# Performance work log

Hardware: AMD Instinct MI355X
Metric: run time of the kernel (lower is better)

## Reference

```python
import jax, jax.numpy as jnp
import numpy as np

DIM = 512
HEADS = 4
DH = 128          # dim_head
CHUNK = 16        # chunk_size
MAX_LR = 0.01     # default_adaptive_step_transform max_lr
EPS = 1e-6        # flax RMSNorm epsilon


def setup_inputs() -> dict:
    key = jax.random.key(0)
    ks = jax.random.split(key, 8)
    B, S = 2, 2048
    dim_inner = HEADS * DH
    seq = jax.random.normal(ks[0], (B, S, DIM), jnp.float32)
    store_norm_scale = jnp.ones((DIM,), jnp.float32)               # RMSNorm scale
    W_kv = (jax.random.normal(ks[1], (DIM, 2 * dim_inner)) * 0.02).astype(jnp.float32)
    W_step = (jax.random.normal(ks[2], (DIM, HEADS)) * 0.02).astype(jnp.float32)
    W_mom = (jax.random.normal(ks[3], (DIM, HEADS)) * 0.02).astype(jnp.float32)
    W_decay = (jax.random.normal(ks[4], (DIM, HEADS)) * 0.02).astype(jnp.float32)
    # past memory-MLP weights, shared init expanded to (b, h, dh, dh)
    w0 = jnp.broadcast_to((jax.random.normal(ks[5], (DH, DH)) * 0.02).astype(jnp.float32), (B, HEADS, DH, DH)) + 0.0
    w1 = jnp.broadcast_to((jax.random.normal(ks[6], (DH, DH)) * 0.02).astype(jnp.float32), (B, HEADS, DH, DH)) + 0.0
    return {"seq": seq, "store_norm_scale": store_norm_scale, "W_kv": W_kv,
            "W_step": W_step, "W_mom": W_mom, "W_decay": W_decay, "w0": w0, "w1": w1}


def _mlp(w0, w1, x):
    # MemoryMLP depth=2: x @ w0 ; silu ; @ w1
    return jax.nn.silu(x @ w0) @ w1


def _chunk_loss(w0, w1, k, lr, v):
    pred = _mlp(w0, w1, k)                       # [c, d]
    return jnp.sum(jnp.mean((pred - v) ** 2, axis=-1) * lr)


def _binop(e1, e2):
    a1, b1 = e1
    a2, b2 = e2
    return a1 * a2, a2 * b1 + b2


def _lin_scan(a, b):
    # first-order linear recurrence y_t = a_t * y_{t-1} + b_t along chunk axis (axis=2)
    return jax.lax.associative_scan(_binop, (a, b), axis=2)[1]


def _store(seq, store_norm_scale, W_kv, W_step, W_mom, W_decay, w0, w1):
    B, S, _ = seq.shape
    n = S // CHUNK
    # pre RMSNorm (with scale)
    x = seq * jax.lax.rsqrt(jnp.mean(seq * seq, axis=-1, keepdims=True) + EPS) * store_norm_scale
    # adaptive per-token lr:  sigmoid(x @ W_step) * max_lr  -> [b, h, s]
    lr = jax.nn.sigmoid(jnp.einsum('bsd,dh->bhs', x, W_step)) * MAX_LR
    # per-chunk mean -> momentum / decay factors  [b, h, n, 1]
    mean = x.reshape(B, n, CHUNK, DIM).mean(axis=2)
    mom = jax.nn.sigmoid(jnp.einsum('bnd,dh->bhn', mean, W_mom))[..., None]
    dec = jax.nn.sigmoid(jnp.einsum('bnd,dh->bhn', mean, W_decay))[..., None]
    # keys / values  [b*h, n, c, dh]
    kv = x @ W_kv
    k, v = jnp.split(kv, 2, axis=-1)
    k = k.reshape(B, n, CHUNK, HEADS, DH).transpose(0, 3, 1, 2, 4).reshape(B * HEADS, n, CHUNK, DH)
    v = v.reshape(B, n, CHUNK, HEADS, DH).transpose(0, 3, 1, 2, 4).reshape(B * HEADS, n, CHUNK, DH)
    lr_ch = lr.reshape(B, HEADS, n, CHUNK).reshape(B * HEADS, n, CHUNK)
    w0bh = w0.reshape(B * HEADS, DH, DH)
    w1bh = w1.reshape(B * HEADS, DH, DH)
    # per-chunk gradients of the MLP loss at the *past* weights (all chunks independent)
    gfn = jax.grad(_chunk_loss, argnums=(0, 1))
    gfn = jax.vmap(gfn, in_axes=(None, None, 0, 0, 0))   # over chunks n
    gfn = jax.vmap(gfn, in_axes=(0, 0, 0, 0, 0))         # over b*h
    g0, g1 = gfn(w0bh, w1bh, k, lr_ch, v)                # [b*h, n, dh, dh]
    s0 = (-g0).reshape(B, HEADS, n, DH * DH)             # surprises
    s1 = (-g1).reshape(B, HEADS, n, DH * DH)
    # momentum scan then decay scan (Titans update rule)
    m0 = _lin_scan(jnp.broadcast_to(mom, s0.shape), s0)
    m1 = _lin_scan(jnp.broadcast_to(mom, s1.shape), s1)
    u0 = _lin_scan(jnp.broadcast_to(1.0 - dec, m0.shape), m0)
    u1 = _lin_scan(jnp.broadcast_to(1.0 - dec, m1.shape), m1)
    updates = jnp.stack([u0.reshape(B, HEADS, n, DH, DH),
                         u1.reshape(B, HEADS, n, DH, DH)], axis=0)  # [2, b, h, n, dh, dh]
    return updates


def reference(seq, store_norm_scale, W_kv, W_step, W_mom, W_decay, w0, w1):
    return _store(seq, store_norm_scale, W_kv, W_step, W_mom, W_decay, w0, w1)
```

## Files before the change

kernel.cpp:

```cpp
#include <hip/hip_runtime.h>

#define DIMX 512
#define HEADSX 4
#define DHX 128
#define CHX 16
#define NCX 128
#define SX 2048
#define BX 2
#define BHX 8
#define PADX 520
#define PADF 136

typedef unsigned short ushort_t;
typedef unsigned int uint_t;
typedef short bf16x8 __attribute__((ext_vector_type(8)));
typedef float f32x4 __attribute__((ext_vector_type(4)));

__device__ __forceinline__ float sigmoidf_(float z){ return 1.0f/(1.0f + __expf(-z)); }

__device__ __forceinline__ ushort_t f2bf(float f){
  uint_t u = __float_as_uint(f);
  return (ushort_t)((u + 0x7FFFu + ((u >> 16) & 1u)) >> 16);
}
__device__ __forceinline__ uint_t pk2(float a, float b){
  return (uint_t)f2bf(a) | ((uint_t)f2bf(b) << 16);
}

__global__ __launch_bounds__(256) void k_rms_lr(const float* __restrict__ seq,
    const float* __restrict__ scale, const float* __restrict__ Wstep,
    float* __restrict__ x, float* __restrict__ lrArr){
  int tok = blockIdx.x; int tid = threadIdx.x;
  const float* row = seq + (size_t)tok*DIMX;
  float v0 = row[tid], v1 = row[tid+256];
  float ss = v0*v0 + v1*v1;
  #pragma unroll
  for (int o=32;o>0;o>>=1) ss += __shfl_down(ss,o,64);
  __shared__ float red[4];
  __shared__ float rs_s;
  int wv = tid>>6, ln = tid&63;
  if (ln==0) red[wv]=ss;
  __syncthreads();
  if (tid==0){
    float ms = (red[0]+red[1]+red[2]+red[3]) * (1.0f/DIMX);
    rs_s = 1.0f/sqrtf(ms + 1e-6f);
  }
  __syncthreads();
  float rs = rs_s;
  float x0 = v0*rs*scale[tid];
  float x1 = v1*rs*scale[tid+256];
  size_t xo = (size_t)tok*DIMX;
  x[xo+tid]=x0; x[xo+tid+256]=x1;
  float a0 = x0*Wstep[tid*4+0] + x1*Wstep[(tid+256)*4+0];
  float a1 = x0*Wstep[tid*4+1] + x1*Wstep[(tid+256)*4+1];
  float a2 = x0*Wstep[tid*4+2] + x1*Wstep[(tid+256)*4+2];
  float a3 = x0*Wstep[tid*4+3] + x1*Wstep[(tid+256)*4+3];
  #pragma unroll
  for (int o=32;o>0;o>>=1){
    a0 += __shfl_down(a0,o,64); a1 += __shfl_down(a1,o,64);
    a2 += __shfl_down(a2,o,64); a3 += __shfl_down(a3,o,64);
  }
  __shared__ float red4[4][4];
  if (ln==0){ red4[wv][0]=a0; red4[wv][1]=a1; red4[wv][2]=a2; red4[wv][3]=a3; }
  __syncthreads();
  if (tid<4){
    float d = red4[0][tid]+red4[1][tid]+red4[2][tid]+red4[3][tid];
    int b = tok>>11, s = tok&2047;
    lrArr[(size_t)(b*HEADSX+tid)*SX + s] = 0.01f * sigmoidf_(d);
  }
}

__global__ __launch_bounds__(64) void k_stats(const float* __restrict__ x,
    const float* __restrict__ Wmom, const float* __restrict__ Wdec,
    float* __restrict__ momw, float* __restrict__ decw){
  int blk = blockIdx.x; int b = blk>>7, nc = blk&127; int ln = threadIdx.x;
  float am[4]={0,0,0,0}, ad[4]={0,0,0,0};
  const float* base = x + ((size_t)(b*SX + nc*CHX))*DIMX;
  for (int r=0;r<8;r++){
    int d = ln + 64*r;
    float m = 0.0f;
    #pragma unroll
    for (int c=0;c<CHX;c++) m += base[(size_t)c*DIMX + d];
    m *= (1.0f/CHX);
    #pragma unroll
    for (int h=0;h<4;h++){ am[h]+=m*Wmom[d*4+h]; ad[h]+=m*Wdec[d*4+h]; }
  }
  #pragma unroll
  for (int h=0;h<4;h++){
    #pragma unroll
    for (int o=32;o>0;o>>=1){ am[h]+=__shfl_down(am[h],o,64); ad[h]+=__shfl_down(ad[h],o,64); }
  }
  if (ln==0){
    #pragma unroll
    for (int h=0;h<4;h++){
      momw[(b*HEADSX+h)*NCX + nc] = sigmoidf_(am[h]);
      decw[(b*HEADSX+h)*NCX + nc] = 1.0f - sigmoidf_(ad[h]);
    }
  }
}

__global__ __launch_bounds__(256) void k_prep(const float* __restrict__ Wkv,
    const float* __restrict__ w0, const float* __restrict__ w1,
    ushort_t* __restrict__ WkvT, ushort_t* __restrict__ w0T,
    ushort_t* __restrict__ w1T, ushort_t* __restrict__ w1n){
  int blk = blockIdx.x; int tid = threadIdx.x;
  if (blk < 64){
    int h = blk >> 4, kt = blk & 15;
    __shared__ ushort_t tile[256][33];
    for (int i=tid; i<8192; i+=256){
      int kk = i >> 8, col = i & 255;
      int wcol = (col < 128) ? (h*128 + col) : (384 + h*128 + col);
      float v = Wkv[(size_t)(kt*32+kk)*1024 + wcol];
      tile[col][kk] = f2bf(v);
    }
    __syncthreads();
    for (int i=tid; i<8192; i+=256){
      int col = i >> 5, kk = i & 31;
      WkvT[(((size_t)h*16 + kt)*256 + col)*32 + kk] = tile[col][kk];
    }
  } else {
    int bh = blk - 64;
    size_t base = (size_t)bh*16384;
    for (int i=tid; i<16384; i+=256){
      int r = i >> 7, c = i & 127;
      w0T[base + i] = f2bf(w0[base + (size_t)c*128 + r]);
      w1T[base + i] = f2bf(w1[base + (size_t)c*128 + r]);
      w1n[base + i] = f2bf(w1[base + i]);
    }
  }
}

__global__ __launch_bounds__(256) void k_fused(const float* __restrict__ x,
    const ushort_t* __restrict__ WkvT, const ushort_t* __restrict__ w0T,
    const ushort_t* __restrict__ w1T, const ushort_t* __restrict__ w1n,
    const float* __restrict__ lrArr,
    ushort_t* __restrict__ fac0, ushort_t* __restrict__ fac1){
  int blk = blockIdx.x;
  int bh = blk & 7, t = blk >> 3;
  int b = bh >> 2, h = bh & 3;
  int bt = bh*NCX + t;
  __shared__ __align__(16) ushort_t xs[16*PADX];
  __shared__ __align__(16) ushort_t ks[16*PADF];
  __shared__ __align__(16) ushort_t as_[16*PADF];
  __shared__ __align__(16) ushort_t dp_[16*PADF];
  __shared__ __align__(16) ushort_t dh_[16*PADF];
  int tid = threadIdx.x;
  int wv = tid>>6, lane = tid&63;
  int quad = lane>>4, nl = lane&15;
  const f32x4 zero = {0.f,0.f,0.f,0.f};

  const float* xb = x + ((size_t)(b*SX + t*CHX))*DIMX;
  #pragma unroll
  for (int it=0; it<8; it++){
    int f = tid + 256*it;
    int c = f >> 7, k4 = f & 127;
    float4 q = ((const float4*)xb)[(size_t)c*128 + k4];
    uint2 u; u.x = pk2(q.x,q.y); u.y = pk2(q.z,q.w);
    *(uint2*)&xs[c*PADX + k4*4] = u;
  }
  __syncthreads();

  f32x4 kacc[2] = {zero, zero};
  f32x4 vacc[2] = {zero, zero};
  const ushort_t* wkvh = WkvT + (size_t)h*16*256*32;
  for (int kt=0; kt<16; kt++){
    bf16x8 Af = *(const bf16x8*)&xs[nl*PADX + kt*32 + quad*8];
    #pragma unroll
    for (int s=0; s<2; s++){
      int ktile = 2*wv + s;
      bf16x8 Bk = *(const bf16x8*)&wkvh[((size_t)kt*256 + (ktile*16+nl))*32 + quad*8];
      kacc[s] = __builtin_amdgcn_mfma_f32_16x16x32_bf16(Af, Bk, kacc[s], 0,0,0);
      int vtile = 8 + 2*wv + s;
      bf16x8 Bv = *(const bf16x8*)&wkvh[((size_t)kt*256 + (vtile*16+nl))*32 + quad*8];
      vacc[s] = __builtin_amdgcn_mfma_f32_16x16x32_bf16(Af, Bv, vacc[s], 0,0,0);
    }
  }
  #pragma unroll
  for (int s=0;s<2;s++){
    #pragma unroll
    for (int r=0;r<4;r++)
      ks[(quad*4+r)*PADF + 32*wv + 16*s + nl] = f2bf(kacc[s][r]);
  }
  __syncthreads();

  const ushort_t* w0b = w0T + (size_t)bh*16384;
  f32x4 hacc[2] = {zero, zero};
  for (int kt=0; kt<4; kt++){
    bf16x8 Af = *(const bf16x8*)&ks[nl*PADF + kt*32 + quad*8];
    #pragma unroll
    for (int s=0; s<2; s++){
      int n0 = (2*wv+s)*16;
      bf16x8 Bf = *(const bf16x8*)&w0b[(size_t)(n0+nl)*128 + kt*32 + quad*8];
      hacc[s] = __builtin_amdgcn_mfma_f32_16x16x32_bf16(Af, Bf, hacc[s], 0,0,0);
    }
  }
  float sp[2][4];
  #pragma unroll
  for (int s=0;s<2;s++){
    #pragma unroll
    for (int r=0;r<4;r++){
      float hh = hacc[s][r];
      float sg = sigmoidf_(hh);
      float a  = hh*sg;
      sp[s][r] = sg*(1.0f + hh*(1.0f-sg));
      as_[(quad*4+r)*PADF + 32*wv + 16*s + nl] = f2bf(a);
    }
  }
  __syncthreads();

  const ushort_t* w1tb = w1T + (size_t)bh*16384;
  f32x4 pacc[2] = {zero, zero};
  for (int kt=0; kt<4; kt++){
    bf16x8 Af = *(const bf16x8*)&as_[nl*PADF + kt*32 + quad*8];
    #pragma unroll
    for (int s=0; s<2; s++){
      int n0 = (2*wv+s)*16;
      bf16x8 Bf = *(const bf16x8*)&w1tb[(size_t)(n0+nl)*128 + kt*32 + quad*8];
      pacc[s] = __builtin_amdgcn_mfma_f32_16x16x32_bf16(Af, Bf, pacc[s], 0,0,0);
    }
  }
  float lrv[4];
  #pragma unroll
  for (int r=0;r<4;r++) lrv[r] = lrArr[(size_t)bh*SX + t*CHX + quad*4 + r];
  #pragma unroll
  for (int s=0;s<2;s++){
    #pragma unroll
    for (int r=0;r<4;r++){
      float dp = (2.0f/DHX)*lrv[r]*(pacc[s][r] - vacc[s][r]);
      dp_[(quad*4+r)*PADF + 32*wv + 16*s + nl] = f2bf(dp);
    }
  }
  __syncthreads();

  const ushort_t* w1nb = w1n + (size_t)bh*16384;
  f32x4 dacc[2] = {zero, zero};
  for (int kt=0; kt<4; kt++){
    bf16x8 Af = *(const bf16x8*)&dp_[nl*PADF + kt*32 + quad*8];
    #pragma unroll
    for (int s=0; s<2; s++){
      int n0 = (2*wv+s)*16;
      bf16x8 Bf = *(const bf16x8*)&w1nb[(size_t)(n0+nl)*128 + kt*32 + quad*8];
      dacc[s] = __builtin_amdgcn_mfma_f32_16x16x32_bf16(Af, Bf, dacc[s], 0,0,0);
    }
  }
  #pragma unroll
  for (int s=0;s<2;s++){
    #pragma unroll
    for (int r=0;r<4;r++)
      dh_[(quad*4+r)*PADF + 32*wv + 16*s + nl] = f2bf(dacc[s][r]*sp[s][r]);
  }
  __syncthreads();

  {
    int p = tid & 127, which = tid >> 7;
    const ushort_t* s0 = which ? dh_ : ks;
    const ushort_t* s1 = which ? dp_ : as_;
    ushort_t rowv[32];
    #pragma unroll
    for (int c=0;c<16;c++){ rowv[c] = s0[c*PADF + p]; rowv[16+c] = s1[c*PADF + p]; }
    ushort_t* dst = (which ? fac1 : fac0) + ((size_t)bt*128 + p)*32;
    const uint4* rv = (const uint4*)rowv;
    uint4* dq = (uint4*)dst;
    dq[0]=rv[0]; dq[1]=rv[1]; dq[2]=rv[2]; dq[3]=rv[3];
  }
}

__global__ __launch_bounds__(64) void k_scan3(const ushort_t* __restrict__ fac0,
    const ushort_t* __restrict__ fac1,
    const float* __restrict__ momw, const float* __restrict__ decw,
    float* __restrict__ out){
  int blk = blockIdx.x;
  int bh  = blk & 7;
  int jb  = (blk >> 3) & 7;
  int ig  = (blk >> 6) & 7;
  int mat = blk >> 9;
  int lane = threadIdx.x;
  int quad = lane >> 4, rrow = lane & 15;
  const f32x4 zero = {0.f,0.f,0.f,0.f};
  const bf16x8 fz = {0,0,0,0,0,0,0,0};

  size_t rowbase = (size_t)bh*NCX*128;
  const ushort_t* pa = fac0 + (rowbase + (size_t)(ig*16 + rrow))*32 + mat*16 + quad*8;
  const ushort_t* pb = fac1 + (rowbase + (size_t)(jb*16 + rrow))*32 + mat*16 + quad*8;
  bool act = (quad < 2);

  bf16x8 fa0=fz, fb0=fz, fa1=fz, fb1=fz;
  if (act){
    fa0 = *(const bf16x8*)(pa);
    fb0 = *(const bf16x8*)(pb);
    fa1 = *(const bf16x8*)(pa + 4096);
    fb1 = *(const bf16x8*)(pb + 4096);
  }

  f32x4 m_ = zero, u_ = zero;
  size_t obase = ((size_t)(mat*BHX + bh)*NCX)*((size_t)DHX*DHX)
               + (size_t)(ig*16 + quad*4)*DHX + (size_t)(jb*16 + rrow);
  const float* mop = momw + bh*NCX;
  const float* dep = decw + bh*NCX;

  for (int t=0; t<NCX; t+=2){
    bf16x8 na0=fz, nb0=fz, na1=fz, nb1=fz;
    if (act && (t+2 < NCX)){
      na0 = *(const bf16x8*)(pa + (size_t)(t+2)*4096);
      nb0 = *(const bf16x8*)(pb + (size_t)(t+2)*4096);
      na1 = *(const bf16x8*)(pa + (size_t)(t+3)*4096);
      nb1 = *(const bf16x8*)(pb + (size_t)(t+3)*4096);
    }
    float mo = mop[t], de = dep[t];
    f32x4 g = __builtin_amdgcn_mfma_f32_16x16x32_bf16(fa0, fb0, zero, 0,0,0);
    float* ob = out + obase + (size_t)t*(DHX*DHX);
    #pragma unroll
    for (int r=0;r<4;r++){
      m_[r] = mo*m_[r] - g[r];
      u_[r] = de*u_[r] + m_[r];
      ob[(size_t)r*DHX] = u_[r];
    }
    mo = mop[t+1]; de = dep[t+1];
    g = __builtin_amdgcn_mfma_f32_16x16x32_bf16(fa1, fb1, zero, 0,0,0);
    ob += (size_t)DHX*DHX;
    #pragma unroll
    for (int r=0;r<4;r++){
      m_[r] = mo*m_[r] - g[r];
      u_[r] = de*u_[r] + m_[r];
      ob[(size_t)r*DHX] = u_[r];
    }
    fa0=na0; fb0=nb0; fa1=na1; fb1=nb1;
  }
}

extern "C" void kernel_launch(void* const* d_in, const int* in_sizes, int n_in,
                              void* d_out, int out_size, void* d_ws, size_t ws_size,
                              hipStream_t stream) {
  (void)in_sizes; (void)n_in; (void)out_size; (void)ws_size;
  const float* seq   = (const float*)d_in[0];
  const float* scale = (const float*)d_in[1];
  const float* Wkv   = (const float*)d_in[2];
  const float* Wstep = (const float*)d_in[3];
  const float* Wmom  = (const float*)d_in[4];
  const float* Wdec  = (const float*)d_in[5];
  const float* w0    = (const float*)d_in[6];
  const float* w1    = (const float*)d_in[7];
  float* out = (float*)d_out;
  float* ws  = (float*)d_ws;

  float*    x     = ws;
  ushort_t* fac0  = (ushort_t*)(ws + 2097152);
  ushort_t* fac1  = (ushort_t*)(ws + 4194304);
  ushort_t* WkvT  = (ushort_t*)(ws + 6291456);
  ushort_t* w0T   = (ushort_t*)(ws + 6553600);
  ushort_t* w1T   = (ushort_t*)(ws + 6619136);
  ushort_t* w1n   = (ushort_t*)(ws + 6684672);
  float*    lrArr = ws + 6750208;
  float*    momw  = ws + 6766592;
  float*    decw  = ws + 6767616;

  k_prep<<<dim3(72), dim3(256), 0, stream>>>(Wkv, w0, w1, WkvT, w0T, w1T, w1n);
  k_rms_lr<<<dim3(BX*SX), dim3(256), 0, stream>>>(seq, scale, Wstep, x, lrArr);
  k_stats<<<dim3(BX*NCX), dim3(64), 0, stream>>>(x, Wmom, Wdec, momw, decw);
  k_fused<<<dim3(BHX*NCX), dim3(256), 0, stream>>>(x, WkvT, w0T, w1T, w1n, lrArr, fac0, fac1);
  k_scan3<<<dim3(1024), dim3(64), 0, stream>>>(fac0, fac1, momw, decw, out);
}
```

Baseline: 246.3 us.

## Fuse RMSNorm, adaptive lr and chunk stats into the main MFMA kernel

Drops the separate RMSNorm/lr kernel and the chunk-statistics kernel. The main fused kernel now reads raw `seq`, computes per-row RMS, the step-lr and the momentum/decay projections with wave reductions, and normalizes while packing to bf16 in LDS. This removes two launches and the fp32 `x` and `lrArr` round trips through global memory. In exchange, each head's block recomputes the row norms and adds extra reductions and a barrier before the GEMM phase.

```diff
diff --git a/kernel.cpp b/kernel.cpp
--- a/kernel.cpp
+++ b/kernel.cpp
@@ -24,78 +24,6 @@
 }
 __device__ __forceinline__ uint_t pk2(float a, float b){
   return (uint_t)f2bf(a) | ((uint_t)f2bf(b) << 16);
-}
-
-__global__ __launch_bounds__(256) void k_rms_lr(const float* __restrict__ seq,
-    const float* __restrict__ scale, const float* __restrict__ Wstep,
-    float* __restrict__ x, float* __restrict__ lrArr){
-  int tok = blockIdx.x; int tid = threadIdx.x;
-  const float* row = seq + (size_t)tok*DIMX;
-  float v0 = row[tid], v1 = row[tid+256];
-  float ss = v0*v0 + v1*v1;
-  #pragma unroll
-  for (int o=32;o>0;o>>=1) ss += __shfl_down(ss,o,64);
-  __shared__ float red[4];
-  __shared__ float rs_s;
-  int wv = tid>>6, ln = tid&63;
-  if (ln==0) red[wv]=ss;
-  __syncthreads();
-  if (tid==0){
-    float ms = (red[0]+red[1]+red[2]+red[3]) * (1.0f/DIMX);
-    rs_s = 1.0f/sqrtf(ms + 1e-6f);
-  }
-  __syncthreads();
-  float rs = rs_s;
-  float x0 = v0*rs*scale[tid];
-  float x1 = v1*rs*scale[tid+256];
-  size_t xo = (size_t)tok*DIMX;
-  x[xo+tid]=x0; x[xo+tid+256]=x1;
-  float a0 = x0*Wstep[tid*4+0] + x1*Wstep[(tid+256)*4+0];
-  float a1 = x0*Wstep[tid*4+1] + x1*Wstep[(tid+256)*4+1];
-  float a2 = x0*Wstep[tid*4+2] + x1*Wstep[(tid+256)*4+2];
-  float a3 = x0*Wstep[tid*4+3] + x1*Wstep[(tid+256)*4+3];
-  #pragma unroll
-  for (int o=32;o>0;o>>=1){
-    a0 += __shfl_down(a0,o,64); a1 += __shfl_down(a1,o,64);
-    a2 += __shfl_down(a2,o,64); a3 += __shfl_down(a3,o,64);
-  }
-  __shared__ float red4[4][4];
-  if (ln==0){ red4[wv][0]=a0; red4[wv][1]=a1; red4[wv][2]=a2; red4[wv][3]=a3; }
-  __syncthreads();
-  if (tid<4){
-    float d = red4[0][tid]+red4[1][tid]+red4[2][tid]+red4[3][tid];
-    int b = tok>>11, s = tok&2047;
-    lrArr[(size_t)(b*HEADSX+tid)*SX + s] = 0.01f * sigmoidf_(d);
-  }
-}
-
-__global__ __launch_bounds__(64) void k_stats(const float* __restrict__ x,
-    const float* __restrict__ Wmom, const float* __restrict__ Wdec,
-    float* __restrict__ momw, float* __restrict__ decw){
-  int blk = blockIdx.x; int b = blk>>7, nc = blk&127; int ln = threadIdx.x;
-  float am[4]={0,0,0,0}, ad[4]={0,0,0,0};
-  const float* base = x + ((size_t)(b*SX + nc*CHX))*DIMX;
-  for (int r=0;r<8;r++){
-    int d = ln + 64*r;
-    float m = 0.0f;
-    #pragma unroll
-    for (int c=0;c<CHX;c++) m += base[(size_t)c*DIMX + d];
-    m *= (1.0f/CHX);
-    #pragma unroll
-    for (int h=0;h<4;h++){ am[h]+=m*Wmom[d*4+h]; ad[h]+=m*Wdec[d*4+h]; }
-  }
-  #pragma unroll
-  for (int h=0;h<4;h++){
-    #pragma unroll
-    for (int o=32;o>0;o>>=1){ am[h]+=__shfl_down(am[h],o,64); ad[h]+=__shfl_down(ad[h],o,64); }
-  }
-  if (ln==0){
-    #pragma unroll
-    for (int h=0;h<4;h++){
-      momw[(b*HEADSX+h)*NCX + nc] = sigmoidf_(am[h]);
-      decw[(b*HEADSX+h)*NCX + nc] = 1.0f - sigmoidf_(ad[h]);
-    }
-  }
 }
 
 __global__ __launch_bounds__(256) void k_prep(const float* __restrict__ Wkv,
@@ -129,11 +57,13 @@
   }
 }
 
-__global__ __launch_bounds__(256) void k_fused(const float* __restrict__ x,
+__global__ __launch_bounds__(256) void k_fused2(const float* __restrict__ seq,
+    const float* __restrict__ scale, const float* __restrict__ Wstep,
+    const float* __restrict__ Wmom, const float* __restrict__ Wdec,
     const ushort_t* __restrict__ WkvT, const ushort_t* __restrict__ w0T,
     const ushort_t* __restrict__ w1T, const ushort_t* __restrict__ w1n,
-    const float* __restrict__ lrArr,
-    ushort_t* __restrict__ fac0, ushort_t* __restrict__ fac1){
+    ushort_t* __restrict__ fac0, ushort_t* __restrict__ fac1,
+    float* __restrict__ momw, float* __restrict__ decw){
   int blk = blockIdx.x;
   int bh = blk & 7, t = blk >> 3;
   int b = bh >> 2, h = bh & 3;
@@ -143,18 +73,70 @@
   __shared__ __align__(16) ushort_t as_[16*PADF];
   __shared__ __align__(16) ushort_t dp_[16*PADF];
   __shared__ __align__(16) ushort_t dh_[16*PADF];
+  __shared__ float red[4][8][4];
+  __shared__ float rs_s[16], lr_s[16];
   int tid = threadIdx.x;
   int wv = tid>>6, lane = tid&63;
   int quad = lane>>4, nl = lane&15;
   const f32x4 zero = {0.f,0.f,0.f,0.f};
 
-  const float* xb = x + ((size_t)(b*SX + t*CHX))*DIMX;
+  const float4* sb = (const float4*)(seq + ((size_t)(b*SX + t*CHX))*DIMX);
+  float4 q[8];
+  #pragma unroll
+  for (int it=0; it<8; it++) q[it] = sb[tid + 256*it];
+  int k4 = tid & 127; int d0 = k4*4;
+  float4 sc4 = *(const float4*)(scale + d0);
+  float wsv[4], wmv[4], wdv[4];
+  #pragma unroll
+  for (int j=0;j<4;j++){
+    wsv[j] = Wstep[(d0+j)*4 + h];
+    wmv[j] = Wmom [(d0+j)*4 + h];
+    wdv[j] = Wdec [(d0+j)*4 + h];
+  }
+  #pragma unroll
+  for (int it=0; it<8; it++){
+    float ssp = q[it].x*q[it].x + q[it].y*q[it].y + q[it].z*q[it].z + q[it].w*q[it].w;
+    float xwx = q[it].x*sc4.x, xwy = q[it].y*sc4.y;
+    float xwz = q[it].z*sc4.z, xww = q[it].w*sc4.w;
+    float lp = xwx*wsv[0] + xwy*wsv[1] + xwz*wsv[2] + xww*wsv[3];
+    float pm = xwx*wmv[0] + xwy*wmv[1] + xwz*wmv[2] + xww*wmv[3];
+    float pd = xwx*wdv[0] + xwy*wdv[1] + xwz*wdv[2] + xww*wdv[3];
+    #pragma unroll
+    for (int o=32;o>0;o>>=1){
+      ssp += __shfl_down(ssp,o,64); lp += __shfl_down(lp,o,64);
+      pm  += __shfl_down(pm,o,64);  pd += __shfl_down(pd,o,64);
+    }
+    if (lane==0){ red[wv][it][0]=ssp; red[wv][it][1]=lp; red[wv][it][2]=pm; red[wv][it][3]=pd; }
+  }
+  __syncthreads();
+  if (tid < 16){
+    int c = tid;
+    int w0i = (c & 1) ? 2 : 0;
+    int iti = c >> 1;
+    float ssc = red[w0i][iti][0] + red[w0i+1][iti][0];
+    float lpc = red[w0i][iti][1] + red[w0i+1][iti][1];
+    float pmc = red[w0i][iti][2] + red[w0i+1][iti][2];
+    float pdc = red[w0i][iti][3] + red[w0i+1][iti][3];
+    float rs = 1.0f / sqrtf(ssc*(1.0f/DIMX) + 1e-6f);
+    rs_s[c] = rs;
+    lr_s[c] = 0.01f * sigmoidf_(rs*lpc);
+    float pmr = rs*pmc, pdr = rs*pdc;
+    #pragma unroll
+    for (int o=8;o>0;o>>=1){ pmr += __shfl_down(pmr,o,16); pdr += __shfl_down(pdr,o,16); }
+    if (c==0){
+      momw[bt] = sigmoidf_(pmr*(1.0f/CHX));
+      decw[bt] = 1.0f - sigmoidf_(pdr*(1.0f/CHX));
+    }
+  }
+  __syncthreads();
   #pragma unroll
   for (int it=0; it<8; it++){
     int f = tid + 256*it;
-    int c = f >> 7, k4 = f & 127;
-    float4 q = ((const float4*)xb)[(size_t)c*128 + k4];
-    uint2 u; u.x = pk2(q.x,q.y); u.y = pk2(q.z,q.w);
+    int c = f >> 7;
+    float rs = rs_s[c];
+    uint2 u;
+    u.x = pk2(q[it].x*rs*sc4.x, q[it].y*rs*sc4.y);
+    u.y = pk2(q[it].z*rs*sc4.z, q[it].w*rs*sc4.w);
     *(uint2*)&xs[c*PADX + k4*4] = u;
   }
   __syncthreads();
@@ -220,7 +202,7 @@
   }
   float lrv[4];
   #pragma unroll
-  for (int r=0;r<4;r++) lrv[r] = lrArr[(size_t)bh*SX + t*CHX + quad*4 + r];
+  for (int r=0;r<4;r++) lrv[r] = lr_s[quad*4 + r];
   #pragma unroll
   for (int s=0;s<2;s++){
     #pragma unroll
@@ -340,22 +322,18 @@
   const float* w0    = (const float*)d_in[6];
   const float* w1    = (const float*)d_in[7];
   float* out = (float*)d_out;
-  float* ws  = (float*)d_ws;
-
-  float*    x     = ws;
-  ushort_t* fac0  = (ushort_t*)(ws + 2097152);
-  ushort_t* fac1  = (ushort_t*)(ws + 4194304);
-  ushort_t* WkvT  = (ushort_t*)(ws + 6291456);
-  ushort_t* w0T   = (ushort_t*)(ws + 6553600);
-  ushort_t* w1T   = (ushort_t*)(ws + 6619136);
-  ushort_t* w1n   = (ushort_t*)(ws + 6684672);
-  float*    lrArr = ws + 6750208;
-  float*    momw  = ws + 6766592;
-  float*    decw  = ws + 6767616;
+
+  ushort_t* fac0 = (ushort_t*)d_ws;
+  ushort_t* fac1 = fac0 + 4194304;
+  ushort_t* WkvT = fac1 + 4194304;
+  ushort_t* w0T  = WkvT + 524288;
+  ushort_t* w1T  = w0T + 131072;
+  ushort_t* w1n  = w1T + 131072;
+  float*    momw = (float*)(w1n + 131072);
+  float*    decw = momw + 1024;
 
   k_prep<<<dim3(72), dim3(256), 0, stream>>>(Wkv, w0, w1, WkvT, w0T, w1T, w1n);
-  k_rms_lr<<<dim3(BX*SX), dim3(256), 0, stream>>>(seq, scale, Wstep, x, lrArr);
-  k_stats<<<dim3(BX*NCX), dim3(64), 0, stream>>>(x, Wmom, Wdec, momw, decw);
-  k_fused<<<dim3(BHX*NCX), dim3(256), 0, stream>>>(x, WkvT, w0T, w1T, w1n, lrArr, fac0, fac1);
+  k_fused2<<<dim3(BHX*NCX), dim3(256), 0, stream>>>(seq, scale, Wstep, Wmom, Wdec,
+      WkvT, w0T, w1T, w1n, fac0, fac1, momw, decw);
   k_scan3<<<dim3(1024), dim3(64), 0, stream>>>(fac0, fac1, momw, decw, out);
 }
```

Result: faster. 233.7 us (-5.1%).
